# Kernel optimization log

Hardware: AMD Instinct MI355X
Metric: run time of the kernel (lower is better)

## Reference

```python
import jax, jax.numpy as jnp
import numpy as np

B, S, H, D = 2, 2048, 16, 64


def setup_inputs() -> dict:
    key = jax.random.key(0)
    kq, kk, kv, km = jax.random.split(key, 4)
    q = jax.random.normal(kq, (B, S, H, D), dtype=jnp.float32)
    k = jax.random.normal(kk, (B, S, H, D), dtype=jnp.float32)
    v = jax.random.normal(kv, (B, S, H, D), dtype=jnp.float32)
    key_padding_mask = jax.random.randint(km, (B, S), 0, 2).astype(bool)
    return {"q": q, "k": k, "v": v, "key_padding_mask": key_padding_mask}


def reference(q, k, v, key_padding_mask):
    # [B,S,H,D] -> [B,H,S,D]; fp32 upcast (inputs already fp32)
    qt = jnp.transpose(q, (0, 2, 1, 3)).astype(jnp.float32)
    kt = jnp.transpose(k, (0, 2, 1, 3)).astype(jnp.float32)
    vt = jnp.transpose(v, (0, 2, 1, 3)).astype(jnp.float32)
    scale = D ** (-0.5)
    # [B,H,Sq,Sk]
    scores = jnp.einsum("bhqd,bhkd->bhqk", qt, kt) * scale
    # masked_fill where key_padding_mask is True -> -inf
    mask = key_padding_mask[:, None, None, :]  # [B,1,1,Sk]
    scores = jnp.where(mask, -jnp.inf, scores)
    attn = jax.nn.softmax(scores, axis=-1)
    out = jnp.einsum("bhqk,bhkd->bhqd", attn, vt).astype(q.dtype)
    # back to [B,S,H,D]
    return jnp.transpose(out, (0, 2, 1, 3))
```

## Files before the change

### kernel.cpp

```cpp
#include <hip/hip_runtime.h>
#include <hip/hip_bf16.h>

#define BB 2
#define SS 2048
#define HH 16
#define DD 64
#define BR 128
#define BC 64
#define NT (SS / BC)
#define NQT (SS / BR)
#define TILE_E (BC * DD)
#define LOG2E 1.44269504f
#define LSTR 72
#define OSZ (BB * SS * HH * DD)
#define LSZ (BB * HH * SS)

typedef __attribute__((ext_vector_type(8))) short short8;
typedef __attribute__((ext_vector_type(4))) float f32x4;
typedef __attribute__((ext_vector_type(16))) float f32x16;
typedef __attribute__((ext_vector_type(4))) unsigned int uint32x4;
typedef __attribute__((ext_vector_type(4))) unsigned short ushort4_t;

static __device__ __forceinline__ unsigned short f2bf(float f) {
    unsigned int u = __float_as_uint(f);
    unsigned int r = u + 0x7FFFu + ((u >> 16) & 1u);
    return (unsigned short)(r >> 16);
}
static __device__ __forceinline__ unsigned int pack2_rn(float a, float b) {
    const unsigned int ua = __float_as_uint(a) + 0x8000u;
    const unsigned int ub = __float_as_uint(b) + 0x8000u;
    return (ua >> 16) | (ub & 0xffff0000u);
}
static __device__ __forceinline__ float fexp2(float x) {
#if __has_builtin(__builtin_amdgcn_exp2f)
    return __builtin_amdgcn_exp2f(x);
#else
    return exp2f(x);
#endif
}
static __device__ __forceinline__ void gl_lds16(const void* g, void* l) {
    __builtin_amdgcn_global_load_lds(
        (const __attribute__((address_space(1))) void*)g,
        (__attribute__((address_space(3))) void*)l, 16, 0, 0);
}

__global__ __launch_bounds__(256, 2)
void prep_kernel(const float* __restrict__ K, const float* __restrict__ V,
                 const int* __restrict__ M,
                 unsigned short* __restrict__ Kb, unsigned short* __restrict__ Vt,
                 int* __restrict__ mcnt)
{
    __shared__ unsigned short Vl[DD * LSTR];

    const int t  = blockIdx.x & (NT - 1);
    const int b  = blockIdx.x >> 9;
    const int bh = blockIdx.x >> 5;
    const int tid = threadIdx.x;
    const size_t tile = (size_t)blockIdx.x * TILE_E;
    const size_t rs = (size_t)HH * DD;
    const float* kb0 = K + (((size_t)b * SS + t * BC) * HH + (bh & 15)) * DD;
    const float* vb0 = V + (((size_t)b * SS + t * BC) * HH + (bh & 15)) * DD;
    const int* mrow = M + (size_t)b * SS + t * BC;

    {
        const int p  = tid & 7;
        const int r0 = tid >> 3;
        #pragma unroll
        for (int half = 0; half < 2; ++half) {
            const int r = r0 + half * 32;
            const int c = p ^ (r & 7);
            const float sel = mrow[r] ? 0.0f : 1.0f;
            const float* ks = kb0 + (size_t)r * rs + c * 8;
            const float4 f0 = *(const float4*)ks;
            const float4 f1 = *(const float4*)(ks + 4);
            short8 o;
            o[0] = (short)f2bf(f0.x * sel); o[1] = (short)f2bf(f0.y * sel);
            o[2] = (short)f2bf(f0.z * sel); o[3] = (short)f2bf(f0.w * sel);
            o[4] = (short)f2bf(f1.x * sel); o[5] = (short)f2bf(f1.y * sel);
            o[6] = (short)f2bf(f1.z * sel); o[7] = (short)f2bf(f1.w * sel);
            *(short8*)(Kb + tile + r * 64 + p * 8) = o;
        }
    }
    {
        const int vr = tid >> 2;
        const int vc = tid & 3;
        const float sel = mrow[vr] ? 0.0f : 1.0f;
        const float* vp = vb0 + (size_t)vr * rs + vc * 16;
        #pragma unroll
        for (int i = 0; i < 4; ++i) {
            const float4 f = *(const float4*)(vp + i * 4);
            const int d = vc * 16 + i * 4;
            Vl[(d + 0) * LSTR + vr] = f2bf(f.x * sel);
            Vl[(d + 1) * LSTR + vr] = f2bf(f.y * sel);
            Vl[(d + 2) * LSTR + vr] = f2bf(f.z * sel);
            Vl[(d + 3) * LSTR + vr] = f2bf(f.w * sel);
        }
    }
    __syncthreads();
    {
        const int p  = tid & 7;
        const int r0 = tid >> 3;
        #pragma unroll
        for (int half = 0; half < 2; ++half) {
            const int r = r0 + half * 32;
            const int c = p ^ (r & 7);
            const short8 o = *(const short8*)&Vl[r * LSTR + c * 8];
            *(short8*)(Vt + tile + r * 64 + p * 8) = o;
        }
    }
    if ((bh & 15) == 0 && tid < 64) {
        const unsigned long long bal = __ballot(mrow[tid] != 0);
        if (tid == 0) mcnt[b * NT + t] = (int)__popcll(bal);
    }
}

template<int NSPLIT>
__global__ __launch_bounds__(256, 2)
void fa3_kernel(const float* __restrict__ Q,
                const unsigned short* __restrict__ Kb,
                const unsigned short* __restrict__ Vt,
                const int* __restrict__ mcnt,
                float* __restrict__ Op,
                float* __restrict__ Lp)
{
    __shared__ __align__(16) unsigned short Ks[2][TILE_E];
    __shared__ __align__(16) unsigned short Vs[2][TILE_E];

    const int blk = blockIdx.x;
    const int qt  = blk & (NQT - 1);
    const int bh  = (blk >> 4) & 31;
    const int spl = blk >> 9;
    const int b   = bh >> 4;
    const int h   = bh & 15;
    const int ktn = NT / NSPLIT;
    const int kt0 = spl * ktn;

    const int tid  = threadIdx.x;
    const int wave = tid >> 6;
    const int lane = tid & 63;
    const int ln   = lane & 31;
    const int l5   = lane >> 5;

    const float qscale = 0.125f * LOG2E;
    const int qrow = qt * BR + wave * 32 + ln;
    const float* qp = Q + (((size_t)b * SS + qrow) * HH + h) * DD;
    short8 qf[4];
    #pragma unroll
    for (int t = 0; t < 4; ++t) {
        const int d0 = t * 16 + l5 * 8;
        const float4 f0 = *(const float4*)(qp + d0);
        const float4 f1 = *(const float4*)(qp + d0 + 4);
        short8 x;
        x[0] = (short)f2bf(f0.x * qscale); x[1] = (short)f2bf(f0.y * qscale);
        x[2] = (short)f2bf(f0.z * qscale); x[3] = (short)f2bf(f0.w * qscale);
        x[4] = (short)f2bf(f1.x * qscale); x[5] = (short)f2bf(f1.y * qscale);
        x[6] = (short)f2bf(f1.z * qscale); x[7] = (short)f2bf(f1.w * qscale);
        qf[t] = x;
    }

    int corr = 0;
    for (int i = 0; i < ktn; ++i) corr += mcnt[b * NT + kt0 + i];

    f32x16 acc0, acc1, zv;
    #pragma unroll
    for (int i = 0; i < 16; ++i) { acc0[i] = 0.f; acc1[i] = 0.f; zv[i] = 0.f; }
    float lsA = 0.f, lsB = 0.f;

    const unsigned short* kb_bh = Kb + (size_t)bh * NT * TILE_E;
    const unsigned short* vt_bh = Vt + (size_t)bh * NT * TILE_E;
    const int we = wave * 1024;
    const int wb = wave * 2048;

    {
        const unsigned short* kbt = kb_bh + (size_t)kt0 * TILE_E;
        const unsigned short* vtt = vt_bh + (size_t)kt0 * TILE_E;
        gl_lds16(kbt + we + lane * 8,       (char*)Ks[0] + wb);
        gl_lds16(kbt + we + 512 + lane * 8, (char*)Ks[0] + wb + 1024);
        gl_lds16(vtt + we + lane * 8,       (char*)Vs[0] + wb);
        gl_lds16(vtt + we + 512 + lane * 8, (char*)Vs[0] + wb + 1024);
    }
    __syncthreads();

    const int pswz = (ln & 7);

    for (int it = 0; it < ktn; ++it) {
        const int cur = it & 1;
        const int nxt = cur ^ 1;
        const int kn = kt0 + ((it + 1 < ktn) ? it + 1 : it);
        const unsigned short* kbt = kb_bh + (size_t)kn * TILE_E;
        const unsigned short* vtt = vt_bh + (size_t)kn * TILE_E;
        gl_lds16(kbt + we + lane * 8,       (char*)Ks[nxt] + wb);
        gl_lds16(kbt + we + 512 + lane * 8, (char*)Ks[nxt] + wb + 1024);
        gl_lds16(vtt + we + lane * 8,       (char*)Vs[nxt] + wb);
        gl_lds16(vtt + we + 512 + lane * 8, (char*)Vs[nxt] + wb + 1024);

        f32x16 s0, s1;
        {
            const int p0 = (0 + l5) ^ pswz;
            const short8 a0 = *(const short8*)(Ks[cur] + ln * 64 + p0 * 8);
            const short8 a1 = *(const short8*)(Ks[cur] + (32 + ln) * 64 + p0 * 8);
            s0 = __builtin_amdgcn_mfma_f32_32x32x16_bf16(a0, qf[0], zv, 0, 0, 0);
            s1 = __builtin_amdgcn_mfma_f32_32x32x16_bf16(a1, qf[0], zv, 0, 0, 0);
        }
        #pragma unroll
        for (int t = 1; t < 4; ++t) {
            const int p = (2 * t + l5) ^ pswz;
            const short8 a0 = *(const short8*)(Ks[cur] + ln * 64 + p * 8);
            const short8 a1 = *(const short8*)(Ks[cur] + (32 + ln) * 64 + p * 8);
            s0 = __builtin_amdgcn_mfma_f32_32x32x16_bf16(a0, qf[t], s0, 0, 0, 0);
            s1 = __builtin_amdgcn_mfma_f32_32x32x16_bf16(a1, qf[t], s1, 0, 0, 0);
        }

        unsigned int pk[2][8];
        #pragma unroll
        for (int hh = 0; hh < 2; ++hh) {
            #pragma unroll
            for (int g = 0; g < 4; ++g) {
                float pv[4];
                #pragma unroll
                for (int j = 0; j < 4; ++j) {
                    const float p = fexp2(hh ? s1[g * 4 + j] : s0[g * 4 + j]);
                    if (hh) lsB += p; else lsA += p;
                    pv[j] = p;
                }
                pk[hh][g * 2 + 0] = pack2_rn(pv[0], pv[1]);
                pk[hh][g * 2 + 1] = pack2_rn(pv[2], pv[3]);
            }
        }

        unsigned int own[2][4], rcv[2][4];
        #pragma unroll
        for (int hh = 0; hh < 2; ++hh) {
            const unsigned int oa0 = l5 ? pk[hh][2] : pk[hh][0];
            const unsigned int oa1 = l5 ? pk[hh][3] : pk[hh][1];
            const unsigned int oa2 = l5 ? pk[hh][6] : pk[hh][4];
            const unsigned int oa3 = l5 ? pk[hh][7] : pk[hh][5];
            const unsigned int sn0 = l5 ? pk[hh][0] : pk[hh][2];
            const unsigned int sn1 = l5 ? pk[hh][1] : pk[hh][3];
            const unsigned int sn2 = l5 ? pk[hh][4] : pk[hh][6];
            const unsigned int sn3 = l5 ? pk[hh][5] : pk[hh][7];
            own[hh][0] = oa0; own[hh][1] = oa1; own[hh][2] = oa2; own[hh][3] = oa3;
            rcv[hh][0] = __shfl_xor(sn0, 32);
            rcv[hh][1] = __shfl_xor(sn1, 32);
            rcv[hh][2] = __shfl_xor(sn2, 32);
            rcv[hh][3] = __shfl_xor(sn3, 32);
        }

        short8 pf[4];
        #pragma unroll
        for (int t = 0; t < 4; ++t) {
            const int hh = t >> 1;
            const int s  = t & 1;
            uint32x4 u;
            u[0] = l5 ? rcv[hh][2 * s + 0] : own[hh][2 * s + 0];
            u[1] = l5 ? rcv[hh][2 * s + 1] : own[hh][2 * s + 1];
            u[2] = l5 ? own[hh][2 * s + 0] : rcv[hh][2 * s + 0];
            u[3] = l5 ? own[hh][2 * s + 1] : rcv[hh][2 * s + 1];
            pf[t] = __builtin_bit_cast(short8, u);
        }

        #pragma unroll
        for (int t = 0; t < 4; ++t) {
            const int p = (2 * t + l5) ^ pswz;
            const short8 vf0 = *(const short8*)(Vs[cur] + ln * 64 + p * 8);
            const short8 vf1 = *(const short8*)(Vs[cur] + (32 + ln) * 64 + p * 8);
            acc0 = __builtin_amdgcn_mfma_f32_32x32x16_bf16(vf0, pf[t], acc0, 0, 0, 0);
            acc1 = __builtin_amdgcn_mfma_f32_32x32x16_bf16(vf1, pf[t], acc1, 0, 0, 0);
        }

        __syncthreads();
    }

    const float lsum = lsA + lsB;
    const float l = lsum + __shfl_xor(lsum, 32) - (float)corr;
    if (NSPLIT > 1) {
        float* op = Op + (size_t)spl * OSZ + (((size_t)b * SS + qrow) * HH + h) * DD;
        #pragma unroll
        for (int dh = 0; dh < 2; ++dh) {
            #pragma unroll
            for (int g = 0; g < 4; ++g) {
                const int d0 = dh * 32 + 8 * g + 4 * l5;
                float4 o;
                o.x = dh ? acc1[g * 4 + 0] : acc0[g * 4 + 0];
                o.y = dh ? acc1[g * 4 + 1] : acc0[g * 4 + 1];
                o.z = dh ? acc1[g * 4 + 2] : acc0[g * 4 + 2];
                o.w = dh ? acc1[g * 4 + 3] : acc0[g * 4 + 3];
                *(float4*)(op + d0) = o;
            }
        }
        if (l5 == 0)
            Lp[spl * LSZ + (b * HH + h) * SS + qrow] = l;
    } else {
        const float inv = 1.0f / l;
        float* op = Op + (((size_t)b * SS + qrow) * HH + h) * DD;
        #pragma unroll
        for (int dh = 0; dh < 2; ++dh) {
            #pragma unroll
            for (int g = 0; g < 4; ++g) {
                const int d0 = dh * 32 + 8 * g + 4 * l5;
                float4 o;
                o.x = (dh ? acc1[g * 4 + 0] : acc0[g * 4 + 0]) * inv;
                o.y = (dh ? acc1[g * 4 + 1] : acc0[g * 4 + 1]) * inv;
                o.z = (dh ? acc1[g * 4 + 2] : acc0[g * 4 + 2]) * inv;
                o.w = (dh ? acc1[g * 4 + 3] : acc0[g * 4 + 3]) * inv;
                *(float4*)(op + d0) = o;
            }
        }
    }
}

__global__ __launch_bounds__(256, 4)
void combine_kernel(const float* __restrict__ Ou, const float* __restrict__ Lp,
                    float* __restrict__ O, int nsplit)
{
    const int gid = blockIdx.x * 256 + threadIdx.x;
    const int i = gid * 4;
    const int b   = i >> 21;
    const int row = (i >> 10) & (SS - 1);
    const int h   = (i >> 6) & (HH - 1);
    const int li  = (b * HH + h) * SS + row;
    float l = 0.f;
    float4 a = {0.f, 0.f, 0.f, 0.f};
    for (int s = 0; s < nsplit; ++s) {
        l += Lp[s * LSZ + li];
        const float4 c = *(const float4*)(Ou + (size_t)s * OSZ + i);
        a.x += c.x; a.y += c.y; a.z += c.z; a.w += c.w;
    }
    const float inv = 1.0f / l;
    float4 o;
    o.x = a.x * inv; o.y = a.y * inv; o.z = a.z * inv; o.w = a.w * inv;
    *(float4*)(O + i) = o;
}

#define KP 72
#define FBR 64
__global__ __launch_bounds__(256, 2)
void fa_fallback(const float* __restrict__ Q, const float* __restrict__ K,
                 const float* __restrict__ V, const int* __restrict__ M,
                 float* __restrict__ O)
{
    __shared__ unsigned short KsF[BC][KP];
    __shared__ unsigned short VsF[DD][KP];
    __shared__ unsigned short PsF[4][16][KP];
    __shared__ float mb[BC];

    const int blk = blockIdx.x;
    const int qt = blk % (SS / FBR);
    const int bh = blk / (SS / FBR);
    const int b = bh / HH;
    const int h = bh % HH;
    const int tid = threadIdx.x;
    const int wave = tid >> 6;
    const int lane = tid & 63;
    const int lq = lane & 15;
    const int quad = lane >> 4;

    const int qrow = qt * FBR + wave * 16 + lq;
    const float* qp = Q + (((size_t)b * SS + qrow) * HH + h) * DD;
    short8 qf[2];
    #pragma unroll
    for (int c = 0; c < 2; ++c) {
        const float4 f0 = *(const float4*)(qp + c * 32 + quad * 8);
        const float4 f1 = *(const float4*)(qp + c * 32 + quad * 8 + 4);
        short8 t;
        t[0] = (short)f2bf(f0.x * 0.125f); t[1] = (short)f2bf(f0.y * 0.125f);
        t[2] = (short)f2bf(f0.z * 0.125f); t[3] = (short)f2bf(f0.w * 0.125f);
        t[4] = (short)f2bf(f1.x * 0.125f); t[5] = (short)f2bf(f1.y * 0.125f);
        t[6] = (short)f2bf(f1.z * 0.125f); t[7] = (short)f2bf(f1.w * 0.125f);
        qf[c] = t;
    }
    f32x4 acc[4];
    #pragma unroll
    for (int dt = 0; dt < 4; ++dt) acc[dt] = (f32x4){0.f, 0.f, 0.f, 0.f};
    float m_i[4] = {-1e30f, -1e30f, -1e30f, -1e30f};
    float l_i[4] = {0.f, 0.f, 0.f, 0.f};

    const int sr = tid >> 2;
    const int sc = tid & 3;
    const size_t rowstride = (size_t)HH * DD;
    const float* kbase = K + (((size_t)b * SS) * HH + h) * DD;
    const float* vbase = V + (((size_t)b * SS) * HH + h) * DD;

    for (int kt = 0; kt < NT; ++kt) {
        const int k0 = kt * BC;
        __syncthreads();
        {
            const float* kp = kbase + (size_t)(k0 + sr) * rowstride + sc * 16;
            #pragma unroll
            for (int i = 0; i < 4; ++i) {
                const float4 f = *(const float4*)(kp + i * 4);
                ushort4_t u;
                u[0] = f2bf(f.x); u[1] = f2bf(f.y); u[2] = f2bf(f.z); u[3] = f2bf(f.w);
                *(ushort4_t*)&KsF[sr][sc * 16 + i * 4] = u;
            }
            const float* vp = vbase + (size_t)(k0 + sr) * rowstride + sc * 16;
            #pragma unroll
            for (int i = 0; i < 4; ++i) {
                const float4 f = *(const float4*)(vp + i * 4);
                const int d = sc * 16 + i * 4;
                VsF[d + 0][sr] = f2bf(f.x); VsF[d + 1][sr] = f2bf(f.y);
                VsF[d + 2][sr] = f2bf(f.z); VsF[d + 3][sr] = f2bf(f.w);
            }
            if (tid < BC) mb[tid] = M[(size_t)b * SS + k0 + tid] ? -1e30f : 0.0f;
        }
        __syncthreads();
        f32x4 s[4];
        #pragma unroll
        for (int ct = 0; ct < 4; ++ct) {
            f32x4 z = (f32x4){0.f, 0.f, 0.f, 0.f};
            const unsigned short* kr = &KsF[ct * 16 + lq][quad * 8];
            const short8 kf0 = *(const short8*)kr;
            const short8 kf1 = *(const short8*)(kr + 32);
            z = __builtin_amdgcn_mfma_f32_16x16x32_bf16(qf[0], kf0, z, 0, 0, 0);
            z = __builtin_amdgcn_mfma_f32_16x16x32_bf16(qf[1], kf1, z, 0, 0, 0);
            s[ct] = z;
        }
        #pragma unroll
        for (int ct = 0; ct < 4; ++ct) {
            const float mbias = mb[ct * 16 + lq];
            s[ct][0] += mbias; s[ct][1] += mbias; s[ct][2] += mbias; s[ct][3] += mbias;
        }
        #pragma unroll
        for (int r = 0; r < 4; ++r) {
            float mx = fmaxf(fmaxf(s[0][r], s[1][r]), fmaxf(s[2][r], s[3][r]));
            mx = fmaxf(mx, __shfl_xor(mx, 1));
            mx = fmaxf(mx, __shfl_xor(mx, 2));
            mx = fmaxf(mx, __shfl_xor(mx, 4));
            mx = fmaxf(mx, __shfl_xor(mx, 8));
            const float m_new = fmaxf(m_i[r], mx);
            const float alpha = __expf(m_i[r] - m_new);
            m_i[r] = m_new;
            float rs = 0.f;
            #pragma unroll
            for (int ct = 0; ct < 4; ++ct) {
                const float p = __expf(s[ct][r] - m_new);
                rs += p;
                PsF[wave][quad * 4 + r][ct * 16 + lq] = f2bf(p);
            }
            rs += __shfl_xor(rs, 1); rs += __shfl_xor(rs, 2);
            rs += __shfl_xor(rs, 4); rs += __shfl_xor(rs, 8);
            l_i[r] = l_i[r] * alpha + rs;
            #pragma unroll
            for (int dt = 0; dt < 4; ++dt) acc[dt][r] *= alpha;
        }
        const unsigned short* pr = &PsF[wave][lq][quad * 8];
        const short8 pf0 = *(const short8*)pr;
        const short8 pf1 = *(const short8*)(pr + 32);
        #pragma unroll
        for (int dt = 0; dt < 4; ++dt) {
            const unsigned short* vr = &VsF[dt * 16 + lq][quad * 8];
            const short8 vf0 = *(const short8*)vr;
            const short8 vf1 = *(const short8*)(vr + 32);
            acc[dt] = __builtin_amdgcn_mfma_f32_16x16x32_bf16(pf0, vf0, acc[dt], 0, 0, 0);
            acc[dt] = __builtin_amdgcn_mfma_f32_16x16x32_bf16(pf1, vf1, acc[dt], 0, 0, 0);
        }
    }
    #pragma unroll
    for (int r = 0; r < 4; ++r) {
        const float inv = 1.0f / l_i[r];
        const int row = qt * FBR + wave * 16 + quad * 4 + r;
        float* op = O + (((size_t)b * SS + row) * HH + h) * DD;
        #pragma unroll
        for (int dt = 0; dt < 4; ++dt)
            op[dt * 16 + lq] = acc[dt][r] * inv;
    }
}

extern "C" void kernel_launch(void* const* d_in, const int* in_sizes, int n_in,
                              void* d_out, int out_size, void* d_ws, size_t ws_size,
                              hipStream_t stream) {
    const float* q = (const float*)d_in[0];
    const float* k = (const float*)d_in[1];
    const float* v = (const float*)d_in[2];
    const int*   m = (const int*)d_in[3];
    float* out = (float*)d_out;

    const int nprep = BB * HH * NT;
    const size_t kb_bytes = (size_t)nprep * TILE_E * 2;
    const size_t mc_bytes = (size_t)BB * NT * 4;

    auto need = [&](int ns) -> size_t {
        return 2 * kb_bytes + (size_t)ns * OSZ * 4 + (size_t)ns * LSZ * 4 + mc_bytes;
    };

    if (ws_size >= need(1) || ws_size >= 2 * kb_bytes + mc_bytes) {
        unsigned short* Kb = (unsigned short*)d_ws;
        unsigned short* Vt = (unsigned short*)((char*)d_ws + kb_bytes);
        char* rest = (char*)d_ws + 2 * kb_bytes;

        int ns = 0;
        if (ws_size >= need(4)) ns = 4;
        else if (ws_size >= need(2)) ns = 2;
        else if (ws_size >= need(1)) ns = 1;

        if (ns >= 2) {
            float* Ou = (float*)rest;
            float* Lp = (float*)(rest + (size_t)ns * OSZ * 4);
            int* mcnt = (int*)(rest + (size_t)ns * OSZ * 4 + (size_t)ns * LSZ * 4);
            prep_kernel<<<nprep, 256, 0, stream>>>(k, v, m, Kb, Vt, mcnt);
            if (ns == 4) {
                fa3_kernel<4><<<4 * BB * HH * NQT, 256, 0, stream>>>(
                    q, Kb, Vt, mcnt, Ou, Lp);
            } else {
                fa3_kernel<2><<<2 * BB * HH * NQT, 256, 0, stream>>>(
                    q, Kb, Vt, mcnt, Ou, Lp);
            }
            combine_kernel<<<OSZ / 4 / 256, 256, 0, stream>>>(Ou, Lp, out, ns);
        } else if (ns == 1) {
            int* mcnt = (int*)rest;
            prep_kernel<<<nprep, 256, 0, stream>>>(k, v, m, Kb, Vt, mcnt);
            fa3_kernel<1><<<BB * HH * NQT, 256, 0, stream>>>(
                q, Kb, Vt, mcnt, out, nullptr);
        } else {
            fa_fallback<<<BB * HH * (SS / FBR), 256, 0, stream>>>(q, k, v, m, out);
        }
    } else {
        fa_fallback<<<BB * HH * (SS / FBR), 256, 0, stream>>>(q, k, v, m, out);
    }
}
```

Measured before the change: 157.0 us.

## Halve attention key tile to 32 columns and raise occupancy to five blocks

The prep kernel now writes K and transposed V as 32-key sub-tiles with matching swizzles. The attention kernel processes 32 keys per iteration with one score MFMA chain instead of two, and uses smaller LDS buffers. Launch bounds rise from 2 to 5 blocks per SIMD group, which cuts registers and LDS per block so more waves can hide latency. The cost is twice as many loop iterations and barriers, and more per-iteration overhead relative to math.

```diff
diff --git a/kernel.cpp b/kernel.cpp
--- a/kernel.cpp
+++ b/kernel.cpp
@@ -6,10 +6,10 @@
 #define HH 16
 #define DD 64
 #define BR 128
-#define BC 64
-#define NT (SS / BC)
+#define NT 32
+#define NT2 64
 #define NQT (SS / BR)
-#define TILE_E (BC * DD)
+#define TILE2_E (32 * DD)
 #define LOG2E 1.44269504f
 #define LSTR 72
 #define OSZ (BB * SS * HH * DD)
@@ -56,11 +56,10 @@
     const int b  = blockIdx.x >> 9;
     const int bh = blockIdx.x >> 5;
     const int tid = threadIdx.x;
-    const size_t tile = (size_t)blockIdx.x * TILE_E;
     const size_t rs = (size_t)HH * DD;
-    const float* kb0 = K + (((size_t)b * SS + t * BC) * HH + (bh & 15)) * DD;
-    const float* vb0 = V + (((size_t)b * SS + t * BC) * HH + (bh & 15)) * DD;
-    const int* mrow = M + (size_t)b * SS + t * BC;
+    const float* kb0 = K + (((size_t)b * SS + t * 64) * HH + (bh & 15)) * DD;
+    const float* vb0 = V + (((size_t)b * SS + t * 64) * HH + (bh & 15)) * DD;
+    const int* mrow = M + (size_t)b * SS + t * 64;
 
     {
         const int p  = tid & 7;
@@ -68,7 +67,7 @@
         #pragma unroll
         for (int half = 0; half < 2; ++half) {
             const int r = r0 + half * 32;
-            const int c = p ^ (r & 7);
+            const int c = p ^ (r0 & 7);
             const float sel = mrow[r] ? 0.0f : 1.0f;
             const float* ks = kb0 + (size_t)r * rs + c * 8;
             const float4 f0 = *(const float4*)ks;
@@ -78,7 +77,8 @@
             o[2] = (short)f2bf(f0.z * sel); o[3] = (short)f2bf(f0.w * sel);
             o[4] = (short)f2bf(f1.x * sel); o[5] = (short)f2bf(f1.y * sel);
             o[6] = (short)f2bf(f1.z * sel); o[7] = (short)f2bf(f1.w * sel);
-            *(short8*)(Kb + tile + r * 64 + p * 8) = o;
+            *(short8*)(Kb + ((size_t)blockIdx.x * 2 + half) * TILE2_E
+                          + r0 * 64 + p * 8) = o;
         }
     }
     {
@@ -98,14 +98,14 @@
     }
     __syncthreads();
     {
-        const int p  = tid & 7;
-        const int r0 = tid >> 3;
-        #pragma unroll
-        for (int half = 0; half < 2; ++half) {
-            const int r = r0 + half * 32;
-            const int c = p ^ (r & 7);
-            const short8 o = *(const short8*)&Vl[r * LSTR + c * 8];
-            *(short8*)(Vt + tile + r * 64 + p * 8) = o;
+        const int rr = tid >> 2;
+        const int p4 = tid & 3;
+        #pragma unroll
+        for (int kh = 0; kh < 2; ++kh) {
+            const int c = p4 ^ (rr & 3);
+            const short8 o = *(const short8*)&Vl[rr * LSTR + kh * 32 + c * 8];
+            *(short8*)(Vt + ((size_t)blockIdx.x * 2 + kh) * TILE2_E
+                          + rr * 32 + p4 * 8) = o;
         }
     }
     if ((bh & 15) == 0 && tid < 64) {
@@ -115,16 +115,16 @@
 }
 
 template<int NSPLIT>
-__global__ __launch_bounds__(256, 2)
-void fa3_kernel(const float* __restrict__ Q,
+__global__ __launch_bounds__(256, 5)
+void fa4_kernel(const float* __restrict__ Q,
                 const unsigned short* __restrict__ Kb,
                 const unsigned short* __restrict__ Vt,
                 const int* __restrict__ mcnt,
                 float* __restrict__ Op,
                 float* __restrict__ Lp)
 {
-    __shared__ __align__(16) unsigned short Ks[2][TILE_E];
-    __shared__ __align__(16) unsigned short Vs[2][TILE_E];
+    __shared__ __align__(16) unsigned short Ks[2][TILE2_E];
+    __shared__ __align__(16) unsigned short Vs[2][TILE2_E];
 
     const int blk = blockIdx.x;
     const int qt  = blk & (NQT - 1);
@@ -132,7 +132,7 @@
     const int spl = blk >> 9;
     const int b   = bh >> 4;
     const int h   = bh & 15;
-    const int ktn = NT / NSPLIT;
+    const int ktn = NT2 / NSPLIT;
     const int kt0 = spl * ktn;
 
     const int tid  = threadIdx.x;
@@ -159,111 +159,83 @@
     }
 
     int corr = 0;
-    for (int i = 0; i < ktn; ++i) corr += mcnt[b * NT + kt0 + i];
+    for (int i = 0; i < ktn / 2; ++i) corr += mcnt[b * NT + (kt0 >> 1) + i];
 
     f32x16 acc0, acc1, zv;
     #pragma unroll
     for (int i = 0; i < 16; ++i) { acc0[i] = 0.f; acc1[i] = 0.f; zv[i] = 0.f; }
     float lsA = 0.f, lsB = 0.f;
 
-    const unsigned short* kb_bh = Kb + (size_t)bh * NT * TILE_E;
-    const unsigned short* vt_bh = Vt + (size_t)bh * NT * TILE_E;
-    const int we = wave * 1024;
-    const int wb = wave * 2048;
-
-    {
-        const unsigned short* kbt = kb_bh + (size_t)kt0 * TILE_E;
-        const unsigned short* vtt = vt_bh + (size_t)kt0 * TILE_E;
-        gl_lds16(kbt + we + lane * 8,       (char*)Ks[0] + wb);
-        gl_lds16(kbt + we + 512 + lane * 8, (char*)Ks[0] + wb + 1024);
-        gl_lds16(vtt + we + lane * 8,       (char*)Vs[0] + wb);
-        gl_lds16(vtt + we + 512 + lane * 8, (char*)Vs[0] + wb + 1024);
-    }
+    const unsigned short* kb_bh = Kb + (size_t)bh * NT2 * TILE2_E;
+    const unsigned short* vt_bh = Vt + (size_t)bh * NT2 * TILE2_E;
+
+    gl_lds16(kb_bh + (size_t)kt0 * TILE2_E + wave * 512 + lane * 8,
+             (char*)Ks[0] + wave * 1024);
+    gl_lds16(vt_bh + (size_t)kt0 * TILE2_E + wave * 512 + lane * 8,
+             (char*)Vs[0] + wave * 1024);
     __syncthreads();
 
-    const int pswz = (ln & 7);
+    const int pswz7 = ln & 7;
+    const int pswz3 = ln & 3;
 
     for (int it = 0; it < ktn; ++it) {
         const int cur = it & 1;
         const int nxt = cur ^ 1;
         const int kn = kt0 + ((it + 1 < ktn) ? it + 1 : it);
-        const unsigned short* kbt = kb_bh + (size_t)kn * TILE_E;
-        const unsigned short* vtt = vt_bh + (size_t)kn * TILE_E;
-        gl_lds16(kbt + we + lane * 8,       (char*)Ks[nxt] + wb);
-        gl_lds16(kbt + we + 512 + lane * 8, (char*)Ks[nxt] + wb + 1024);
-        gl_lds16(vtt + we + lane * 8,       (char*)Vs[nxt] + wb);
-        gl_lds16(vtt + we + 512 + lane * 8, (char*)Vs[nxt] + wb + 1024);
-
-        f32x16 s0, s1;
+        gl_lds16(kb_bh + (size_t)kn * TILE2_E + wave * 512 + lane * 8,
+                 (char*)Ks[nxt] + wave * 1024);
+        gl_lds16(vt_bh + (size_t)kn * TILE2_E + wave * 512 + lane * 8,
+                 (char*)Vs[nxt] + wave * 1024);
+
+        f32x16 s0;
         {
-            const int p0 = (0 + l5) ^ pswz;
-            const short8 a0 = *(const short8*)(Ks[cur] + ln * 64 + p0 * 8);
-            const short8 a1 = *(const short8*)(Ks[cur] + (32 + ln) * 64 + p0 * 8);
-            s0 = __builtin_amdgcn_mfma_f32_32x32x16_bf16(a0, qf[0], zv, 0, 0, 0);
-            s1 = __builtin_amdgcn_mfma_f32_32x32x16_bf16(a1, qf[0], zv, 0, 0, 0);
+            const int p = l5 ^ pswz7;
+            const short8 kf = *(const short8*)(Ks[cur] + ln * 64 + p * 8);
+            s0 = __builtin_amdgcn_mfma_f32_32x32x16_bf16(kf, qf[0], zv, 0, 0, 0);
         }
         #pragma unroll
         for (int t = 1; t < 4; ++t) {
-            const int p = (2 * t + l5) ^ pswz;
-            const short8 a0 = *(const short8*)(Ks[cur] + ln * 64 + p * 8);
-            const short8 a1 = *(const short8*)(Ks[cur] + (32 + ln) * 64 + p * 8);
-            s0 = __builtin_amdgcn_mfma_f32_32x32x16_bf16(a0, qf[t], s0, 0, 0, 0);
-            s1 = __builtin_amdgcn_mfma_f32_32x32x16_bf16(a1, qf[t], s1, 0, 0, 0);
-        }
-
-        unsigned int pk[2][8];
-        #pragma unroll
-        for (int hh = 0; hh < 2; ++hh) {
-            #pragma unroll
-            for (int g = 0; g < 4; ++g) {
-                float pv[4];
-                #pragma unroll
-                for (int j = 0; j < 4; ++j) {
-                    const float p = fexp2(hh ? s1[g * 4 + j] : s0[g * 4 + j]);
-                    if (hh) lsB += p; else lsA += p;
-                    pv[j] = p;
-                }
-                pk[hh][g * 2 + 0] = pack2_rn(pv[0], pv[1]);
-                pk[hh][g * 2 + 1] = pack2_rn(pv[2], pv[3]);
-            }
-        }
-
-        unsigned int own[2][4], rcv[2][4];
-        #pragma unroll
-        for (int hh = 0; hh < 2; ++hh) {
-            const unsigned int oa0 = l5 ? pk[hh][2] : pk[hh][0];
-            const unsigned int oa1 = l5 ? pk[hh][3] : pk[hh][1];
-            const unsigned int oa2 = l5 ? pk[hh][6] : pk[hh][4];
-            const unsigned int oa3 = l5 ? pk[hh][7] : pk[hh][5];
-            const unsigned int sn0 = l5 ? pk[hh][0] : pk[hh][2];
-            const unsigned int sn1 = l5 ? pk[hh][1] : pk[hh][3];
-            const unsigned int sn2 = l5 ? pk[hh][4] : pk[hh][6];
-            const unsigned int sn3 = l5 ? pk[hh][5] : pk[hh][7];
-            own[hh][0] = oa0; own[hh][1] = oa1; own[hh][2] = oa2; own[hh][3] = oa3;
-            rcv[hh][0] = __shfl_xor(sn0, 32);
-            rcv[hh][1] = __shfl_xor(sn1, 32);
-            rcv[hh][2] = __shfl_xor(sn2, 32);
-            rcv[hh][3] = __shfl_xor(sn3, 32);
-        }
-
-        short8 pf[4];
-        #pragma unroll
-        for (int t = 0; t < 4; ++t) {
-            const int hh = t >> 1;
-            const int s  = t & 1;
+            const int p = (2 * t + l5) ^ pswz7;
+            const short8 kf = *(const short8*)(Ks[cur] + ln * 64 + p * 8);
+            s0 = __builtin_amdgcn_mfma_f32_32x32x16_bf16(kf, qf[t], s0, 0, 0, 0);
+        }
+
+        unsigned int pk[8];
+        #pragma unroll
+        for (int g = 0; g < 4; ++g) {
+            float pv[4];
+            #pragma unroll
+            for (int j = 0; j < 4; ++j) {
+                const float p = fexp2(s0[g * 4 + j]);
+                if (g & 2) lsB += p; else lsA += p;
+                pv[j] = p;
+            }
+            pk[g * 2 + 0] = pack2_rn(pv[0], pv[1]);
+            pk[g * 2 + 1] = pack2_rn(pv[2], pv[3]);
+        }
+
+        short8 pf[2];
+        #pragma unroll
+        for (int t = 0; t < 2; ++t) {
+            const unsigned int x0 = pk[4 * t + 0], x1 = pk[4 * t + 1];
+            const unsigned int y0 = pk[4 * t + 2], y1 = pk[4 * t + 3];
+            const unsigned int s0w = l5 ? x0 : y0;
+            const unsigned int s1w = l5 ? x1 : y1;
+            const unsigned int r0 = __shfl_xor(s0w, 32);
+            const unsigned int r1 = __shfl_xor(s1w, 32);
             uint32x4 u;
-            u[0] = l5 ? rcv[hh][2 * s + 0] : own[hh][2 * s + 0];
-            u[1] = l5 ? rcv[hh][2 * s + 1] : own[hh][2 * s + 1];
-            u[2] = l5 ? own[hh][2 * s + 0] : rcv[hh][2 * s + 0];
-            u[3] = l5 ? own[hh][2 * s + 1] : rcv[hh][2 * s + 1];
+            u[0] = l5 ? r0 : x0;
+            u[1] = l5 ? r1 : x1;
+            u[2] = l5 ? y0 : r0;
+            u[3] = l5 ? y1 : r1;
             pf[t] = __builtin_bit_cast(short8, u);
         }
 
         #pragma unroll
-        for (int t = 0; t < 4; ++t) {
-            const int p = (2 * t + l5) ^ pswz;
-            const short8 vf0 = *(const short8*)(Vs[cur] + ln * 64 + p * 8);
-            const short8 vf1 = *(const short8*)(Vs[cur] + (32 + ln) * 64 + p * 8);
+        for (int t = 0; t < 2; ++t) {
+            const int p = (2 * t + l5) ^ pswz3;
+            const short8 vf0 = *(const short8*)(Vs[cur] + ln * 32 + p * 8);
+            const short8 vf1 = *(const short8*)(Vs[cur] + (32 + ln) * 32 + p * 8);
             acc0 = __builtin_amdgcn_mfma_f32_32x32x16_bf16(vf0, pf[t], acc0, 0, 0, 0);
             acc1 = __builtin_amdgcn_mfma_f32_32x32x16_bf16(vf1, pf[t], acc1, 0, 0, 0);
         }
@@ -339,10 +311,10 @@
                  const float* __restrict__ V, const int* __restrict__ M,
                  float* __restrict__ O)
 {
-    __shared__ unsigned short KsF[BC][KP];
+    __shared__ unsigned short KsF[64][KP];
     __shared__ unsigned short VsF[DD][KP];
     __shared__ unsigned short PsF[4][16][KP];
-    __shared__ float mb[BC];
+    __shared__ float mb[64];
 
     const int blk = blockIdx.x;
     const int qt = blk % (SS / FBR);
@@ -382,7 +354,7 @@
     const float* vbase = V + (((size_t)b * SS) * HH + h) * DD;
 
     for (int kt = 0; kt < NT; ++kt) {
-        const int k0 = kt * BC;
+        const int k0 = kt * 64;
         __syncthreads();
         {
             const float* kp = kbase + (size_t)(k0 + sr) * rowstride + sc * 16;
@@ -401,7 +373,7 @@
                 VsF[d + 0][sr] = f2bf(f.x); VsF[d + 1][sr] = f2bf(f.y);
                 VsF[d + 2][sr] = f2bf(f.z); VsF[d + 3][sr] = f2bf(f.w);
             }
-            if (tid < BC) mb[tid] = M[(size_t)b * SS + k0 + tid] ? -1e30f : 0.0f;
+            if (tid < 64) mb[tid] = M[(size_t)b * SS + k0 + tid] ? -1e30f : 0.0f;
         }
         __syncthreads();
         f32x4 s[4];
@@ -476,14 +448,14 @@
     float* out = (float*)d_out;
 
     const int nprep = BB * HH * NT;
-    const size_t kb_bytes = (size_t)nprep * TILE_E * 2;
+    const size_t kb_bytes = (size_t)BB * HH * NT2 * TILE2_E * 2;
     const size_t mc_bytes = (size_t)BB * NT * 4;
 
     auto need = [&](int ns) -> size_t {
         return 2 * kb_bytes + (size_t)ns * OSZ * 4 + (size_t)ns * LSZ * 4 + mc_bytes;
     };
 
-    if (ws_size >= need(1) || ws_size >= 2 * kb_bytes + mc_bytes) {
+    if (ws_size >= 2 * kb_bytes + mc_bytes) {
         unsigned short* Kb = (unsigned short*)d_ws;
         unsigned short* Vt = (unsigned short*)((char*)d_ws + kb_bytes);
         char* rest = (char*)d_ws + 2 * kb_bytes;
@@ -499,17 +471,17 @@
             int* mcnt = (int*)(rest + (size_t)ns * OSZ * 4 + (size_t)ns * LSZ * 4);
             prep_kernel<<<nprep, 256, 0, stream>>>(k, v, m, Kb, Vt, mcnt);
             if (ns == 4) {
-                fa3_kernel<4><<<4 * BB * HH * NQT, 256, 0, stream>>>(
+                fa4_kernel<4><<<4 * BB * HH * NQT, 256, 0, stream>>>(
                     q, Kb, Vt, mcnt, Ou, Lp);
             } else {
-                fa3_kernel<2><<<2 * BB * HH * NQT, 256, 0, stream>>>(
+                fa4_kernel<2><<<2 * BB * HH * NQT, 256, 0, stream>>>(
                     q, Kb, Vt, mcnt, Ou, Lp);
             }
             combine_kernel<<<OSZ / 4 / 256, 256, 0, stream>>>(Ou, Lp, out, ns);
         } else if (ns == 1) {
             int* mcnt = (int*)rest;
             prep_kernel<<<nprep, 256, 0, stream>>>(k, v, m, Kb, Vt, mcnt);
-            fa3_kernel<1><<<BB * HH * NQT, 256, 0, stream>>>(
+            fa4_kernel<1><<<BB * HH * NQT, 256, 0, stream>>>(
                 q, Kb, Vt, mcnt, out, nullptr);
         } else {
             fa_fallback<<<BB * HH * (SS / FBR), 256, 0, stream>>>(q, k, v, m, out);
```

Measured after the change: 168.9 us. 1.08x slower.
